# Kernel tuning notes

Measured on AMD Instinct MI355X. Metric: run time of the kernel, lower is better.

## Reference

```python
import jax, jax.numpy as jnp
import numpy as np

MARGIN = 0.3
WARMUP_EPOCHS = 10
K = 5
ALPHA = 2.0
SAME_CAM_NEG_BOOST = 1.2
NEG_INF = jnp.float32(-jnp.inf)
POS_INF = jnp.float32(jnp.inf)


def setup_inputs() -> dict:
    key = jax.random.key(0)
    k1, k2, k3 = jax.random.split(key, 3)
    N, D = 8192, 2048
    feats = jax.random.normal(k1, (N, D), dtype=jnp.float32)
    labels = jax.random.randint(k2, (N,), 0, 256, dtype=jnp.int64)
    camids = jax.random.randint(k3, (N,), 0, 8, dtype=jnp.int64)
    return {"feats": feats, "labels": labels, "camids": camids, "epoch": 20}


def _topk_mean(dist_mat, mask, k, largest):
    # dist_mat [N,N], mask [N,N] bool. Per-row mean of k largest/smallest valid elems.
    if largest:
        work = jnp.where(mask, dist_mat, NEG_INF)
        vals, _ = jax.lax.top_k(work, k)            # [N,k] largest
        fallback = jnp.max(work, axis=1)
    else:
        work = jnp.where(mask, dist_mat, POS_INF)
        vals = -jax.lax.top_k(-work, k)[0]          # [N,k] smallest
        fallback = jnp.min(work, axis=1)
    is_valid = jnp.isfinite(vals)
    safe_sum = jnp.sum(jnp.where(is_valid, vals, 0.0), axis=1)
    counts = jnp.maximum(is_valid.sum(axis=1), 1)
    mean = safe_sum / counts
    return jnp.where(is_valid.any(axis=1), mean, fallback)


def _forward(feats, labels, camids, epoch):
    # (1) L2 normalize
    norm = jnp.linalg.norm(feats, axis=-1, keepdims=True)
    x = feats / jnp.maximum(norm, 1e-12)
    # Euclidean distance matrix [N,N]
    sq = jnp.sum(x * x, axis=1)
    dist2 = sq[:, None] + sq[None, :] - 2.0 * (x @ x.T)
    dist = jnp.sqrt(jnp.maximum(dist2, 1e-12))
    # masks (constants w.r.t. grad)
    N = feats.shape[0]
    eye = jnp.eye(N, dtype=bool)
    same_label = labels[:, None] == labels[None, :]
    same_cam = camids[:, None] == camids[None, :]
    is_pos = same_label & ~eye & ~same_cam   # cross_cam_pos=True
    is_neg = ~same_label & ~eye
    # boosted same-camera negatives
    neg_bias = jnp.where(is_neg & same_cam, SAME_CAM_NEG_BOOST, 1.0)
    dist_neg_sel = dist / jnp.maximum(neg_bias, 1e-6)
    # (2) top-k hard mining
    d_ap = _topk_mean(dist, is_pos, K, largest=True)
    d_an = _topk_mean(dist_neg_sel, is_neg, K, largest=False)
    # (5) hardness-aware weighting (no grad)
    w = jax.lax.stop_gradient(jax.nn.sigmoid(ALPHA * (d_ap - d_an)))
    w = w / jnp.maximum(w.mean(), 1e-12)
    # (3) margin schedule
    if epoch is not None and epoch < WARMUP_EPOCHS:
        per_sample = jax.nn.softplus(-(d_an - d_ap))
    else:
        per_sample = jax.nn.relu(d_ap - d_an + MARGIN)  # MarginRankingLoss, y=1
    loss = jnp.mean(w * per_sample)
    return loss, jax.lax.stop_gradient(d_ap), jax.lax.stop_gradient(d_an)


def reference(feats, labels, camids, epoch):
    return _forward(feats, labels, camids, epoch)
```

## Files before the change

kernel.cpp:

```cpp
#include <hip/hip_runtime.h>
#include <hip/hip_bf16.h>
#include <stdint.h>

typedef float   floatx4  __attribute__((ext_vector_type(4)));
typedef int     intx4    __attribute__((ext_vector_type(4)));
typedef int     intx8    __attribute__((ext_vector_type(8)));
typedef _Float16 halfx8  __attribute__((ext_vector_type(8)));
typedef _Float16 halfx4  __attribute__((ext_vector_type(4)));
typedef _Float16 half2v  __attribute__((ext_vector_type(2)));
typedef short   short2v  __attribute__((ext_vector_type(2)));
typedef unsigned short ushort8 __attribute__((ext_vector_type(8)));

#define NROW 8192
#define NDIM 2048
#define BM 128
#define BKB 128
#define NSTRIP 64
#define NOFF (NSTRIP*(NSTRIP-1)/2)
#define NTILE (NSTRIP*(NSTRIP+1)/2)
#define DT_LD 136
#define KL_SYM 64
#define SLOT_P 8
#define MERGE_BLOCKS 256

__device__ __forceinline__ void ins_desc(float (&a)[5], float v) {
#pragma unroll
    for (int k = 0; k < 5; ++k) { float hi = fmaxf(a[k], v); float lo = fminf(a[k], v); a[k] = hi; v = lo; }
}
__device__ __forceinline__ void ins_asc(float (&a)[5], float v) {
#pragma unroll
    for (int k = 0; k < 5; ++k) { float lo = fminf(a[k], v); float hi = fmaxf(a[k], v); a[k] = lo; v = hi; }
}

__device__ __forceinline__ int   h2bits(half2v v) { return __builtin_bit_cast(int, v); }
__device__ __forceinline__ half2v bits2h(int v)   { return __builtin_bit_cast(half2v, v); }
__device__ __forceinline__ int bfi(int m, int a, int b) { return (m & a) | (~m & b); }
__device__ __forceinline__ int nzmask16(int v) {
    short2v s = __builtin_bit_cast(short2v, v);
    short2v n = (short2v)(0) - s;
    int o = v | __builtin_bit_cast(int, n);
    short2v m = __builtin_bit_cast(short2v, o) >> 15;
    return __builtin_bit_cast(int, m);
}
__device__ __forceinline__ int nzmask16_small(int v) {
    short2v s = __builtin_bit_cast(short2v, v);
    short2v n = (short2v)(0) - s;
    short2v m = n >> 15;
    return __builtin_bit_cast(int, m);
}
__device__ __forceinline__ void ins_desc2(half2v (&a)[5], half2v v) {
#pragma unroll
    for (int k = 0; k < 5; ++k) {
        half2v hi = __builtin_elementwise_max(a[k], v);
        half2v lo = __builtin_elementwise_min(a[k], v);
        a[k] = hi; v = lo;
    }
}
__device__ __forceinline__ void ins_asc2(half2v (&a)[5], half2v v) {
#pragma unroll
    for (int k = 0; k < 5; ++k) {
        half2v lo = __builtin_elementwise_min(a[k], v);
        half2v hi = __builtin_elementwise_max(a[k], v);
        a[k] = lo; v = hi;
    }
}

__device__ __forceinline__ void load_lds16(const void* g, void* l) {
    __builtin_amdgcn_global_load_lds((__attribute__((address_space(1))) void*)(void*)g,
                                     (__attribute__((address_space(3))) void*)l,
                                     16, 0, 0);
}

__global__ __launch_bounds__(256) void k_normalize(const float* __restrict__ feats,
                                                   unsigned char* __restrict__ xb,
                                                   float* __restrict__ sq) {
    const int lane = threadIdx.x & 63;
    const int row = (blockIdx.x << 2) + (threadIdx.x >> 6);
    const float* f = feats + (size_t)row * NDIM;
    float4 v[8];
    float ss = 0.f;
#pragma unroll
    for (int i = 0; i < 8; ++i) {
        v[i] = *(const float4*)(f + ((i << 6) + lane) * 4);
        ss += v[i].x * v[i].x + v[i].y * v[i].y + v[i].z * v[i].z + v[i].w * v[i].w;
    }
#pragma unroll
    for (int o = 32; o > 0; o >>= 1) ss += __shfl_xor(ss, o);
    float inv = 1.0f / fmaxf(sqrtf(ss), 1e-12f);
    if (lane == 0) sq[row] = ss * inv * inv;
    unsigned char* xo = xb + (size_t)row * NDIM;
#pragma unroll
    for (int i = 0; i < 8; ++i) {
        int w0 = __builtin_amdgcn_cvt_pk_fp8_f32(v[i].x * inv, v[i].y * inv, 0, false);
        w0     = __builtin_amdgcn_cvt_pk_fp8_f32(v[i].z * inv, v[i].w * inv, w0, true);
        *(int*)(xo + ((i << 6) + lane) * 4) = w0;
    }
}

__device__ __forceinline__ void scan_half_row(const _Float16* Dt_,
        const unsigned short* labcam_cols,
        int srow, int shalf, int pli, float (&pos5)[5], float (&neg5)[5]) {
    const int jb = shalf * 64;
    const int s2 = 2 * (srow & 7);
    const int pli2 = pli * 0x00010001;
    const int ONE2  = 0x3C003C00;
    const int BOOST2= 0x398E398E;
    const int PINF2 = 0x7C007C00;
    const int NINF2 = 0xFC00FC00;
    half2v p5[5], n5[5];
#pragma unroll
    for (int k = 0; k < 5; ++k) { p5[k] = bits2h(NINF2); n5[k] = bits2h(PINF2); }
#pragma unroll
    for (int c8 = 0; c8 < 8; ++c8) {
        const int pc = ((shalf * 8 + c8) + s2) & 15;
        intx4 v  = *(const intx4*)(Dt_ + srow * DT_LD + pc * 8);
        intx4 lc = *(const intx4*)(labcam_cols + jb + c8 * 8);
#pragma unroll
        for (int e = 0; e < 4; ++e) {
            const int d2p = v[e];
            const int x   = pli2 ^ lc[e];
            const int mdl = nzmask16(x & 0xFFF0FFF0);
            const int mdc = nzmask16_small(x & 0x000F000F);
            const int mul = bfi(mdc, ONE2, BOOST2);
            half2v nv = bits2h(d2p) * bits2h(mul);
            nv = bits2h(bfi(mdl, h2bits(nv), PINF2));
            ins_asc2(n5, nv);
            const int pmask = mdc & ~mdl;
            half2v pv = bits2h(bfi(pmask, d2p, NINF2));
            half2v chk = __builtin_elementwise_max(pv, p5[4]);
            if (h2bits(chk) != h2bits(p5[4])) ins_desc2(p5, pv);
        }
    }
    half2v tp[5], tn[5];
#pragma unroll
    for (int k = 0; k < 5; ++k) {
        tp[k] = bits2h((int)__builtin_amdgcn_alignbit((unsigned)h2bits(p5[k]), (unsigned)h2bits(p5[k]), 16));
        tn[k] = bits2h((int)__builtin_amdgcn_alignbit((unsigned)h2bits(n5[k]), (unsigned)h2bits(n5[k]), 16));
    }
#pragma unroll
    for (int k = 0; k < 5; ++k) { ins_desc2(p5, tp[k]); ins_asc2(n5, tn[k]); }
#pragma unroll
    for (int k = 0; k < 5; ++k) { pos5[k] = (float)p5[k][0]; neg5[k] = (float)n5[k][0]; }
}

__device__ __forceinline__ void emit_lists(float (&pos5)[5], float (&neg5)[5], int shalf,
        _Float16* posp, _Float16* negp, int gi, int slot) {
    float tp[5], tn[5];
#pragma unroll
    for (int k = 0; k < 5; ++k) { tp[k] = __shfl_xor(pos5[k], 1); tn[k] = __shfl_xor(neg5[k], 1); }
#pragma unroll
    for (int k = 0; k < 5; ++k) {
        if (tp[k] > pos5[4]) ins_desc(pos5, tp[k]);
        if (tn[k] < neg5[4]) ins_asc(neg5, tn[k]);
    }
    if (shalf == 0) {
        const float NINF = -__builtin_inff(), PINF = __builtin_inff();
        halfx8 hp, hn;
#pragma unroll
        for (int k = 0; k < 5; ++k) { hp[k] = (_Float16)pos5[k]; hn[k] = (_Float16)neg5[k]; }
        hp[5] = hp[6] = hp[7] = (_Float16)NINF;
        hn[5] = hn[6] = hn[7] = (_Float16)PINF;
        const size_t off = ((size_t)slot * NROW + gi) * SLOT_P;
        *(halfx8*)(posp + off) = hp;
        *(halfx8*)(negp + off) = hn;
    }
}

__global__ __launch_bounds__(256, 2) void k_gemm_sym(
        const unsigned char* __restrict__ xb, const float* __restrict__ sq,
        const int* __restrict__ labels, const int* __restrict__ camids,
        _Float16* __restrict__ posp, _Float16* __restrict__ negp) {
    __shared__ __align__(16) char smem[65536 + 2048];
    _Float16* Dt = (_Float16*)smem;
    float* sqr_s = (float*)(smem + 65536);
    float* sqc_s = sqr_s + BM;
    unsigned short* labcam_a = (unsigned short*)(sqc_s + BM);
    unsigned short* labcam_b = labcam_a + BM;

    const int tid = threadIdx.x;
    const int w = tid >> 6, lane = tid & 63;
    const int wm = w >> 1, wn = w & 1;

    int a, b;
    {
        int bx = blockIdx.x;
        if (bx < NOFF) {
            a = (int)((1.0f + sqrtf(8.0f * (float)bx + 1.0f)) * 0.5f);
            while (a * (a - 1) / 2 > bx) --a;
            while (a * (a + 1) / 2 <= bx) ++a;
            b = bx - a * (a - 1) / 2;
        } else {
            a = b = bx - NOFF;
        }
    }
    const int r0 = a * BM, c0 = b * BM;

    const int lr = lane >> 3;
    const int lc = ((lane & 7) ^ lr) * 16;

    auto stage = [&](int buf, int kkv) {
        char* Asb = smem + (buf << 15);
        char* Bsb = Asb + 16384;
#pragma unroll
        for (int q = 0; q < 4; ++q) {
            const int ra = w * 32 + q * 8;
            load_lds16(xb + (size_t)(r0 + ra + lr) * NDIM + kkv + lc, Asb + ra * BKB);
            load_lds16(xb + (size_t)(c0 + ra + lr) * NDIM + kkv + lc, Bsb + ra * BKB);
        }
    };

    stage(0, 0);

    if (tid < BM) {
        int gi = r0 + tid;
        sqr_s[tid] = sq[gi];
        labcam_a[tid] = (unsigned short)((labels[gi] << 4) | camids[gi]);
    } else {
        int t2 = tid - BM;
        int gj = c0 + t2;
        sqc_s[t2] = sq[gj];
        labcam_b[t2] = (unsigned short)((labels[gj] << 4) | camids[gj]);
    }

    const int srow = tid >> 1;
    const int shalf = tid & 1;

    const int m16 = lane & 15;
    const int quad = lane >> 4;
    const int s7 = m16 & 7;
    const int pc0 = ((2 * quad) ^ s7) * 16;
    const int pc1 = ((2 * quad + 1) ^ s7) * 16;

    floatx4 acc[4][4];
#pragma unroll
    for (int mi = 0; mi < 4; ++mi)
#pragma unroll
        for (int ni = 0; ni < 4; ++ni) {
            floatx4 z = {0.f, 0.f, 0.f, 0.f};
            acc[mi][ni] = z;
        }

    __syncthreads();

    for (int t = 0; t < 16; ++t) {
        const int cur = t & 1;
        if (t < 15) stage(cur ^ 1, (t + 1) * BKB);
        const char* Ab = smem + (cur << 15);
        const char* Bb = Ab + 16384;
        intx8 bfr[4];
#pragma unroll
        for (int ni = 0; ni < 4; ++ni) {
            const char* bp = Bb + (wn * 64 + ni * 16 + m16) * BKB;
            intx4 lo = *(const intx4*)(bp + pc0);
            intx4 hi = *(const intx4*)(bp + pc1);
            bfr[ni] = __builtin_shufflevector(lo, hi, 0, 1, 2, 3, 4, 5, 6, 7);
        }
        __builtin_amdgcn_s_setprio(1);
#pragma unroll
        for (int mi = 0; mi < 4; ++mi) {
            const char* ap = Ab + (wm * 64 + mi * 16 + m16) * BKB;
            intx4 lo = *(const intx4*)(ap + pc0);
            intx4 hi = *(const intx4*)(ap + pc1);
            intx8 af = __builtin_shufflevector(lo, hi, 0, 1, 2, 3, 4, 5, 6, 7);
#pragma unroll
            for (int ni = 0; ni < 4; ++ni)
                acc[mi][ni] = __builtin_amdgcn_mfma_scale_f32_16x16x128_f8f6f4(
                    af, bfr[ni], acc[mi][ni], 0, 0, 0, 127, 0, 127);
        }
        __builtin_amdgcn_s_setprio(0);
        __syncthreads();
    }

#pragma unroll
    for (int mi = 0; mi < 4; ++mi) {
        const int il = wm * 64 + mi * 16 + quad * 4;
#pragma unroll
        for (int ni = 0; ni < 4; ++ni) {
            const int jl = wn * 64 + ni * 16 + m16;
            const float sj = sqc_s[jl];
#pragma unroll
            for (int r = 0; r < 4; ++r) {
                float d2 = fmaxf(sqr_s[il + r] + sj - 2.0f * acc[mi][ni][r], 1e-12f);
                const int pch = (((jl >> 3) + 2 * ((il + r) & 7)) & 15);
                Dt[(il + r) * DT_LD + (pch << 3) + (jl & 7)] = (_Float16)d2;
            }
        }
    }
    __syncthreads();

    float pos5[5], neg5[5];
    scan_half_row(Dt, labcam_b, srow, shalf, (int)labcam_a[srow], pos5, neg5);
    emit_lists(pos5, neg5, shalf, posp, negp, r0 + srow, b);

    if (a != b) {
        __syncthreads();
#pragma unroll
        for (int ni = 0; ni < 4; ++ni) {
            const int jl = wn * 64 + ni * 16 + m16;
            const float sj = sqc_s[jl];
            const int cw2 = 2 * (jl & 7);
#pragma unroll
            for (int mi = 0; mi < 4; ++mi) {
                const int il = wm * 64 + mi * 16 + quad * 4;
                halfx4 h;
#pragma unroll
                for (int r = 0; r < 4; ++r)
                    h[r] = (_Float16)fmaxf(sqr_s[il + r] + sj - 2.0f * acc[mi][ni][r], 1e-12f);
                const int pch = (((il >> 3) + cw2) & 15);
                *(halfx4*)(Dt + jl * DT_LD + (pch << 3) + (il & 7)) = h;
            }
        }
        __syncthreads();
        scan_half_row(Dt, labcam_a, srow, shalf, (int)labcam_b[srow], pos5, neg5);
        emit_lists(pos5, neg5, shalf, posp, negp, c0 + srow, a);
    }
}

__global__ __launch_bounds__(256) void k_merge_sym(const _Float16* __restrict__ posp,
        const _Float16* __restrict__ negp, const int* __restrict__ epoch_p,
        float* __restrict__ out, float* __restrict__ wsum_p, float* __restrict__ wpsum_p) {
    const int t = threadIdx.x;
    const int rl = t & 31;
    const int sg = t >> 5;
    const int row = blockIdx.x * 32 + rl;
    const float NINF = -__builtin_inff(), PINF = __builtin_inff();
    float p5[5] = {NINF, NINF, NINF, NINF, NINF};
    float n5[5] = {PINF, PINF, PINF, PINF, PINF};
    const size_t rbase = (size_t)row * SLOT_P;
#pragma unroll
    for (int s = 0; s < 8; ++s) {
        const size_t off = (size_t)(sg * 8 + s) * ((size_t)NROW * SLOT_P) + rbase;
        halfx8 pv = *(const halfx8*)(posp + off);
        halfx8 nv = *(const halfx8*)(negp + off);
#pragma unroll
        for (int e = 0; e < 8; ++e) { float f = (float)pv[e]; if (f > p5[4]) ins_desc(p5, f); }
#pragma unroll
        for (int e = 0; e < 8; ++e) { float f = (float)nv[e]; if (f < n5[4]) ins_asc(n5, f); }
    }
    __shared__ __align__(16) _Float16 lp[32][8][8];
    __shared__ __align__(16) _Float16 ln[32][8][8];
    const int sw = (sg + rl) & 7;
    {
        halfx8 hp, hn;
#pragma unroll
        for (int k = 0; k < 5; ++k) { hp[k] = (_Float16)p5[k]; hn[k] = (_Float16)n5[k]; }
        hp[5] = hp[6] = hp[7] = (_Float16)NINF;
        hn[5] = hn[6] = hn[7] = (_Float16)PINF;
        *(halfx8*)&lp[rl][sw][0] = hp;
        *(halfx8*)&ln[rl][sw][0] = hn;
    }
    __syncthreads();
    if (t < 32) {
        float P5[5] = {NINF, NINF, NINF, NINF, NINF};
        float N5[5] = {PINF, PINF, PINF, PINF, PINF};
#pragma unroll
        for (int g = 0; g < 8; ++g) {
            halfx8 pv = *(const halfx8*)&lp[t][g][0];
            halfx8 nv = *(const halfx8*)&ln[t][g][0];
#pragma unroll
            for (int e = 0; e < 8; ++e) { float f = (float)pv[e]; if (f > P5[4]) ins_desc(P5, f); }
#pragma unroll
            for (int e = 0; e < 8; ++e) { float f = (float)nv[e]; if (f < N5[4]) ins_asc(N5, f); }
        }
        float s = 0.f; int c = 0;
#pragma unroll
        for (int k = 0; k < 5; ++k) { bool fin = (P5[k] > NINF); s += fin ? sqrtf(P5[k]) : 0.f; c += fin ? 1 : 0; }
        float d_ap = (c > 0) ? s / (float)c : NINF;
        s = 0.f; c = 0;
#pragma unroll
        for (int k = 0; k < 5; ++k) { bool fin = (N5[k] < PINF); s += fin ? sqrtf(N5[k]) : 0.f; c += fin ? 1 : 0; }
        float d_an = (c > 0) ? s / (float)c : PINF;

        const int orow = blockIdx.x * 32 + t;
        out[1 + orow] = d_ap;
        out[1 + NROW + orow] = d_an;
        float diff = d_ap - d_an;
        float w0 = 1.0f / (1.0f + expf(-2.0f * diff));
        float p;
        if (*epoch_p < 10) {
            p = fmaxf(diff, 0.0f) + log1pf(expf(-fabsf(diff)));
        } else {
            p = fmaxf(diff + 0.3f, 0.0f);
        }
        float wp = w0 * p;
#pragma unroll
        for (int o = 16; o > 0; o >>= 1) { w0 += __shfl_down(w0, o, 32); wp += __shfl_down(wp, o, 32); }
        if (t == 0) { wsum_p[blockIdx.x] = w0; wpsum_p[blockIdx.x] = wp; }
    }
}

__global__ void k_finalize(const float* __restrict__ wsum_p, const float* __restrict__ wpsum_p,
                           float* __restrict__ out) {
    const int t = threadIdx.x;
    float sw  = wsum_p[t] + wsum_p[t + 64] + wsum_p[t + 128] + wsum_p[t + 192];
    float swp = wpsum_p[t] + wpsum_p[t + 64] + wpsum_p[t + 128] + wpsum_p[t + 192];
#pragma unroll
    for (int o = 32; o > 0; o >>= 1) { sw += __shfl_down(sw, o); swp += __shfl_down(swp, o); }
    if (t == 0) {
        float M = fmaxf(sw / (float)NROW, 1e-12f);
        out[0] = swp / ((float)NROW * M);
    }
}

extern "C" void kernel_launch(void* const* d_in, const int* in_sizes, int n_in,
                              void* d_out, int out_size, void* d_ws, size_t ws_size,
                              hipStream_t stream) {
    const float* feats  = (const float*)d_in[0];
    const int*   labels = (const int*)d_in[1];
    const int*   camids = (const int*)d_in[2];
    const int*   epoch  = (const int*)d_in[3];
    float* out = (float*)d_out;
    char* ws = (char*)d_ws;

    unsigned char* xb = (unsigned char*)ws;
    float* sq = (float*)(ws + 16777216);
    const size_t LIST_HALVES = (size_t)KL_SYM * NROW * SLOT_P;
    _Float16* posp = (_Float16*)(ws + 16777216 + 32768);
    _Float16* negp = posp + LIST_HALVES;
    float* wsum_p  = (float*)((char*)(posp + 2 * LIST_HALVES));
    float* wpsum_p = wsum_p + MERGE_BLOCKS;

    k_normalize<<<NROW / 4, 256, 0, stream>>>(feats, xb, sq);
    k_gemm_sym<<<NTILE, 256, 0, stream>>>(xb, sq, labels, camids, posp, negp);
    k_merge_sym<<<MERGE_BLOCKS, 256, 0, stream>>>(posp, negp, epoch, out, wsum_p, wpsum_p);
    k_finalize<<<1, 64, 0, stream>>>(wsum_p, wpsum_p, out);
}
```

Before: 242.8 us.

## Switch GEMM to 32x32x64 FP8 MFMA with smaller K slices and remapped tiles

Replaces the 16x16x128 scaled MFMA tiles with 32x32x64 tiles, halves the K slice to 64 bytes so the double-buffered LDS staging shrinks to 32KB, and raises launch bounds to 3 blocks per CU for higher occupancy. The block-to-tile mapping is also permuted by interleaving blockIdx across eight groups, which may improve L2 locality or load spread. The cost is twice as many K iterations and barriers, plus a new LDS swizzle and epilogue index mapping that must match the 32x32 accumulator layout.

```diff
diff --git a/kernel.cpp b/kernel.cpp
--- a/kernel.cpp
+++ b/kernel.cpp
@@ -3,6 +3,7 @@
 #include <stdint.h>
 
 typedef float   floatx4  __attribute__((ext_vector_type(4)));
+typedef float   floatx16 __attribute__((ext_vector_type(16)));
 typedef int     intx4    __attribute__((ext_vector_type(4)));
 typedef int     intx8    __attribute__((ext_vector_type(8)));
 typedef _Float16 halfx8  __attribute__((ext_vector_type(8)));
@@ -14,7 +15,8 @@
 #define NROW 8192
 #define NDIM 2048
 #define BM 128
-#define BKB 128
+#define SLICE 64
+#define NSLICE 32
 #define NSTRIP 64
 #define NOFF (NSTRIP*(NSTRIP-1)/2)
 #define NTILE (NSTRIP*(NSTRIP+1)/2)
@@ -166,13 +168,13 @@
     }
 }
 
-__global__ __launch_bounds__(256, 2) void k_gemm_sym(
+__global__ __launch_bounds__(256, 3) void k_gemm_sym(
         const unsigned char* __restrict__ xb, const float* __restrict__ sq,
         const int* __restrict__ labels, const int* __restrict__ camids,
         _Float16* __restrict__ posp, _Float16* __restrict__ negp) {
-    __shared__ __align__(16) char smem[65536 + 2048];
+    __shared__ __align__(16) char smem[36864];
     _Float16* Dt = (_Float16*)smem;
-    float* sqr_s = (float*)(smem + 65536);
+    float* sqr_s = (float*)(smem + 34816);
     float* sqc_s = sqr_s + BM;
     unsigned short* labcam_a = (unsigned short*)(sqc_s + BM);
     unsigned short* labcam_b = labcam_a + BM;
@@ -184,28 +186,31 @@
     int a, b;
     {
         int bx = blockIdx.x;
-        if (bx < NOFF) {
-            a = (int)((1.0f + sqrtf(8.0f * (float)bx + 1.0f)) * 0.5f);
-            while (a * (a - 1) / 2 > bx) --a;
-            while (a * (a + 1) / 2 <= bx) ++a;
-            b = bx - a * (a - 1) / 2;
+        int orig;
+        if (bx < NOFF) orig = (bx & 7) * (NOFF / 8) + (bx >> 3);
+        else orig = bx;
+        if (orig < NOFF) {
+            a = (int)((1.0f + sqrtf(8.0f * (float)orig + 1.0f)) * 0.5f);
+            while (a * (a - 1) / 2 > orig) --a;
+            while (a * (a + 1) / 2 <= orig) ++a;
+            b = orig - a * (a - 1) / 2;
         } else {
-            a = b = bx - NOFF;
+            a = b = orig - NOFF;
         }
     }
     const int r0 = a * BM, c0 = b * BM;
 
-    const int lr = lane >> 3;
-    const int lc = ((lane & 7) ^ lr) * 16;
-
-    auto stage = [&](int buf, int kkv) {
-        char* Asb = smem + (buf << 15);
-        char* Bsb = Asb + 16384;
-#pragma unroll
-        for (int q = 0; q < 4; ++q) {
-            const int ra = w * 32 + q * 8;
-            load_lds16(xb + (size_t)(r0 + ra + lr) * NDIM + kkv + lc, Asb + ra * BKB);
-            load_lds16(xb + (size_t)(c0 + ra + lr) * NDIM + kkv + lc, Bsb + ra * BKB);
+    const int lr = lane >> 2;
+    const int lc = (((lane & 3) - ((lane >> 3) & 3)) & 3) * 16;
+
+    auto stage = [&](int buf, int koff) {
+        char* Asb = smem + (buf << 14);
+        char* Bsb = Asb + 8192;
+#pragma unroll
+        for (int q = 0; q < 2; ++q) {
+            const int ra = w * 32 + q * 16;
+            load_lds16(xb + (size_t)(r0 + ra + lr) * NDIM + koff + lc, Asb + ra * SLICE);
+            load_lds16(xb + (size_t)(c0 + ra + lr) * NDIM + koff + lc, Bsb + ra * SLICE);
         }
     };
 
@@ -225,64 +230,63 @@
     const int srow = tid >> 1;
     const int shalf = tid & 1;
 
-    const int m16 = lane & 15;
-    const int quad = lane >> 4;
-    const int s7 = m16 & 7;
-    const int pc0 = ((2 * quad) ^ s7) * 16;
-    const int pc1 = ((2 * quad + 1) ^ s7) * 16;
-
-    floatx4 acc[4][4];
-#pragma unroll
-    for (int mi = 0; mi < 4; ++mi)
-#pragma unroll
-        for (int ni = 0; ni < 4; ++ni) {
-            floatx4 z = {0.f, 0.f, 0.f, 0.f};
-            acc[mi][ni] = z;
-        }
+    const int m32 = lane & 31;
+    const int hi = lane >> 5;
+    const int key = (lane >> 1) & 3;
+    const int p0 = ((2 * hi + key) & 3) * 16;
+    const int p1 = ((2 * hi + 1 + key) & 3) * 16;
+
+    floatx16 acc[2][2];
+#pragma unroll
+    for (int ti = 0; ti < 2; ++ti)
+#pragma unroll
+        for (int tj = 0; tj < 2; ++tj)
+#pragma unroll
+            for (int r = 0; r < 16; ++r) acc[ti][tj][r] = 0.f;
 
     __syncthreads();
 
-    for (int t = 0; t < 16; ++t) {
-        const int cur = t & 1;
-        if (t < 15) stage(cur ^ 1, (t + 1) * BKB);
-        const char* Ab = smem + (cur << 15);
-        const char* Bb = Ab + 16384;
-        intx8 bfr[4];
-#pragma unroll
-        for (int ni = 0; ni < 4; ++ni) {
-            const char* bp = Bb + (wn * 64 + ni * 16 + m16) * BKB;
-            intx4 lo = *(const intx4*)(bp + pc0);
-            intx4 hi = *(const intx4*)(bp + pc1);
-            bfr[ni] = __builtin_shufflevector(lo, hi, 0, 1, 2, 3, 4, 5, 6, 7);
+    for (int s = 0; s < NSLICE; ++s) {
+        const int cur = s & 1;
+        if (s < NSLICE - 1) stage(cur ^ 1, (s + 1) * SLICE);
+        const char* Ab = smem + (cur << 14);
+        const char* Bb = Ab + 8192;
+        intx8 bf[2];
+#pragma unroll
+        for (int tj = 0; tj < 2; ++tj) {
+            const char* bp = Bb + (wn * 64 + tj * 32 + m32) * SLICE;
+            intx4 lo = *(const intx4*)(bp + p0);
+            intx4 hi4 = *(const intx4*)(bp + p1);
+            bf[tj] = __builtin_shufflevector(lo, hi4, 0, 1, 2, 3, 4, 5, 6, 7);
         }
         __builtin_amdgcn_s_setprio(1);
 #pragma unroll
-        for (int mi = 0; mi < 4; ++mi) {
-            const char* ap = Ab + (wm * 64 + mi * 16 + m16) * BKB;
-            intx4 lo = *(const intx4*)(ap + pc0);
-            intx4 hi = *(const intx4*)(ap + pc1);
-            intx8 af = __builtin_shufflevector(lo, hi, 0, 1, 2, 3, 4, 5, 6, 7);
-#pragma unroll
-            for (int ni = 0; ni < 4; ++ni)
-                acc[mi][ni] = __builtin_amdgcn_mfma_scale_f32_16x16x128_f8f6f4(
-                    af, bfr[ni], acc[mi][ni], 0, 0, 0, 127, 0, 127);
+        for (int ti = 0; ti < 2; ++ti) {
+            const char* ap = Ab + (wm * 64 + ti * 32 + m32) * SLICE;
+            intx4 lo = *(const intx4*)(ap + p0);
+            intx4 hi4 = *(const intx4*)(ap + p1);
+            intx8 af = __builtin_shufflevector(lo, hi4, 0, 1, 2, 3, 4, 5, 6, 7);
+            acc[ti][0] = __builtin_amdgcn_mfma_scale_f32_32x32x64_f8f6f4(
+                af, bf[0], acc[ti][0], 0, 0, 0, 127, 0, 127);
+            acc[ti][1] = __builtin_amdgcn_mfma_scale_f32_32x32x64_f8f6f4(
+                af, bf[1], acc[ti][1], 0, 0, 0, 127, 0, 127);
         }
         __builtin_amdgcn_s_setprio(0);
         __syncthreads();
     }
 
 #pragma unroll
-    for (int mi = 0; mi < 4; ++mi) {
-        const int il = wm * 64 + mi * 16 + quad * 4;
-#pragma unroll
-        for (int ni = 0; ni < 4; ++ni) {
-            const int jl = wn * 64 + ni * 16 + m16;
+    for (int ti = 0; ti < 2; ++ti) {
+#pragma unroll
+        for (int tj = 0; tj < 2; ++tj) {
+            const int jl = wn * 64 + tj * 32 + m32;
             const float sj = sqc_s[jl];
 #pragma unroll
-            for (int r = 0; r < 4; ++r) {
-                float d2 = fmaxf(sqr_s[il + r] + sj - 2.0f * acc[mi][ni][r], 1e-12f);
-                const int pch = (((jl >> 3) + 2 * ((il + r) & 7)) & 15);
-                Dt[(il + r) * DT_LD + (pch << 3) + (jl & 7)] = (_Float16)d2;
+            for (int r = 0; r < 16; ++r) {
+                const int il = wm * 64 + ti * 32 + (r & 3) + 8 * (r >> 2) + 4 * hi;
+                float d2 = fmaxf(sqr_s[il] + sj - 2.0f * acc[ti][tj][r], 1e-12f);
+                const int pch = (((jl >> 3) + 2 * (il & 7)) & 15);
+                Dt[il * DT_LD + (pch << 3) + (jl & 7)] = (_Float16)d2;
             }
         }
     }
@@ -295,19 +299,24 @@
     if (a != b) {
         __syncthreads();
 #pragma unroll
-        for (int ni = 0; ni < 4; ++ni) {
-            const int jl = wn * 64 + ni * 16 + m16;
-            const float sj = sqc_s[jl];
-            const int cw2 = 2 * (jl & 7);
-#pragma unroll
-            for (int mi = 0; mi < 4; ++mi) {
-                const int il = wm * 64 + mi * 16 + quad * 4;
-                halfx4 h;
-#pragma unroll
-                for (int r = 0; r < 4; ++r)
-                    h[r] = (_Float16)fmaxf(sqr_s[il + r] + sj - 2.0f * acc[mi][ni][r], 1e-12f);
-                const int pch = (((il >> 3) + cw2) & 15);
-                *(halfx4*)(Dt + jl * DT_LD + (pch << 3) + (il & 7)) = h;
+        for (int tj = 0; tj < 2; ++tj) {
+#pragma unroll
+            for (int ti = 0; ti < 2; ++ti) {
+                const int jl = wn * 64 + tj * 32 + m32;
+                const float sj = sqc_s[jl];
+                const int cw2 = 2 * (jl & 7);
+#pragma unroll
+                for (int rq = 0; rq < 4; ++rq) {
+                    const int base_row = wm * 64 + ti * 32 + 8 * rq + 4 * hi;
+                    halfx4 h;
+#pragma unroll
+                    for (int e = 0; e < 4; ++e) {
+                        const int il = base_row + e;
+                        h[e] = (_Float16)fmaxf(sqr_s[il] + sj - 2.0f * acc[ti][tj][rq * 4 + e], 1e-12f);
+                    }
+                    const int pch = (((base_row >> 3) + cw2) & 15);
+                    *(halfx4*)(Dt + jl * DT_LD + (pch << 3) + 4 * hi) = h;
+                }
             }
         }
         __syncthreads();
```

Result: no change. 245.3 us (+1.0%).
